# Performance work log

Hardware: AMD Instinct MI355X
Metric: run time of the kernel (lower is better)

## Reference

```python
import jax, jax.numpy as jnp
import numpy as np

B, T, V, D, F, L, H = 2, 1024, 50257, 768, 3072, 6, 12
HD = D // H
EPS = 1e-5


def setup_inputs() -> dict:
    key = jax.random.key(0)
    ks = jax.random.split(key, 8)
    s = 0.02
    return {
        "idx": jax.random.randint(ks[0], (B, T), 0, V),
        "tok_emb": jax.random.normal(ks[1], (V, D), jnp.float32) * s,
        "pos_emb": jax.random.normal(ks[2], (T, D), jnp.float32) * s,
        "ln1_w": jnp.ones((L, D), jnp.float32),
        "ln1_b": jnp.zeros((L, D), jnp.float32),
        "qkv_w": jax.random.normal(ks[3], (L, 3 * D, D), jnp.float32) * s,
        "qkv_b": jnp.zeros((L, 3 * D), jnp.float32),
        "out_w": jax.random.normal(ks[4], (L, D, D), jnp.float32) * s,
        "out_b": jnp.zeros((L, D), jnp.float32),
        "ln2_w": jnp.ones((L, D), jnp.float32),
        "ln2_b": jnp.zeros((L, D), jnp.float32),
        "fc1_w": jax.random.normal(ks[5], (L, F, D), jnp.float32) * s,
        "fc1_b": jnp.zeros((L, F), jnp.float32),
        "fc2_w": jax.random.normal(ks[6], (L, D, F), jnp.float32) * s,
        "fc2_b": jnp.zeros((L, D), jnp.float32),
        "lnf_w": jnp.ones((D,), jnp.float32),
        "lnf_b": jnp.zeros((D,), jnp.float32),
    }


def _ln(x, w, b):
    m = x.mean(-1, keepdims=True)
    v = ((x - m) ** 2).mean(-1, keepdims=True)
    return (x - m) * jax.lax.rsqrt(v + EPS) * w + b


def reference(idx, tok_emb, pos_emb, ln1_w, ln1_b, qkv_w, qkv_b, out_w, out_b,
              ln2_w, ln2_b, fc1_w, fc1_b, fc2_w, fc2_b, lnf_w, lnf_b):
    b, t = idx.shape
    x = tok_emb[idx] + pos_emb[:t]  # (B,T,D)
    mask = jnp.tril(jnp.ones((t, t), bool))
    scale = HD ** -0.5

    def block(x, p):
        l1w, l1b, qw, qb, ow, ob, l2w, l2b, f1w, f1b, f2w, f2b = p
        h = _ln(x, l1w, l1b)
        qkv = h @ qw.T + qb                     # (B,T,3D)
        q, k, v = jnp.split(qkv, 3, axis=-1)
        q = q.reshape(b, t, H, HD).transpose(0, 2, 1, 3)  # (B,H,T,HD)
        k = k.reshape(b, t, H, HD).transpose(0, 2, 1, 3)
        v = v.reshape(b, t, H, HD).transpose(0, 2, 1, 3)
        attn = jnp.einsum('bhqd,bhkd->bhqk', q, k) * scale
        attn = jnp.where(mask, attn, -jnp.inf)
        attn = jax.nn.softmax(attn, axis=-1)
        o = jnp.einsum('bhqk,bhkd->bhqd', attn, v)
        o = o.transpose(0, 2, 1, 3).reshape(b, t, D)
        x = x + o @ ow.T + ob
        h = _ln(x, l2w, l2b)
        x = x + jax.nn.gelu(h @ f1w.T + f1b, approximate=False) @ f2w.T + f2b
        return x, None

    x, _ = jax.lax.scan(block, x, (ln1_w, ln1_b, qkv_w, qkv_b, out_w, out_b,
                                   ln2_w, ln2_b, fc1_w, fc1_b, fc2_w, fc2_b))
    x = _ln(x, lnf_w, lnf_b)
    logits = x @ tok_emb.T  # weight-tied head, (B,T,V)
    return logits
```

## Files before the change

kernel.cpp:

```cpp
#include <hip/hip_runtime.h>
#include <hip/hip_bf16.h>

typedef __attribute__((ext_vector_type(8))) short short8;
typedef __attribute__((ext_vector_type(4))) float f32x4;
typedef __attribute__((ext_vector_type(4))) unsigned short u16x4;

#define DEVI static __device__ __forceinline__

constexpr int TT  = 1024;
constexpr int DD  = 768;
constexpr int FF  = 3072;
constexpr int VV  = 50257;
constexpr int VP  = 50304;
constexpr int HH  = 12;
constexpr int BTOT = 2048;

DEVI unsigned short f2bf(float f) {
    unsigned int u = __builtin_bit_cast(unsigned int, f);
    u += 0x7fffu + ((u >> 16) & 1u);
    return (unsigned short)(u >> 16);
}
DEVI float bf2f(unsigned short h) {
    unsigned int u = ((unsigned int)h) << 16;
    return __builtin_bit_cast(float, u);
}
DEVI f32x4 mfma16(short8 a, short8 b, f32x4 c) {
    return __builtin_amdgcn_mfma_f32_16x16x32_bf16(a, b, c, 0, 0, 0);
}

__global__ __launch_bounds__(256) void cvt4_k(const float* __restrict__ s,
                                              unsigned short* __restrict__ d, long n4) {
    long i = (long)blockIdx.x * 256 + threadIdx.x;
    if (i >= n4) return;
    float4 v = ((const float4*)s)[i];
    u16x4 o;
    o[0] = f2bf(v.x); o[1] = f2bf(v.y); o[2] = f2bf(v.z); o[3] = f2bf(v.w);
    ((u16x4*)d)[i] = o;
}

__global__ __launch_bounds__(192) void pad_tok_k(const float* __restrict__ s,
                                                 unsigned short* __restrict__ d) {
    int r = blockIdx.x;
    int c = threadIdx.x * 4;
    u16x4 o = {0, 0, 0, 0};
    if (r < VV) {
        float4 v = *(const float4*)(s + (size_t)r * DD + c);
        o[0] = f2bf(v.x); o[1] = f2bf(v.y); o[2] = f2bf(v.z); o[3] = f2bf(v.w);
    }
    *(u16x4*)(d + (size_t)r * DD + c) = o;
}

__global__ __launch_bounds__(256) void embed_k(const int* __restrict__ idx,
                                               const float* __restrict__ tok,
                                               const float* __restrict__ pos,
                                               float* __restrict__ x) {
    int row = blockIdx.x;
    int t = row & (TT - 1);
    int id = idx[row];
    for (int c = threadIdx.x; c < DD; c += 256)
        x[(size_t)row * DD + c] = tok[(size_t)id * DD + c] + pos[(size_t)t * DD + c];
}

__global__ __launch_bounds__(256) void ln_k(const float* __restrict__ x,
                                            const float* __restrict__ w,
                                            const float* __restrict__ b,
                                            unsigned short* __restrict__ out) {
    int row = blockIdx.x;
    const float* xr = x + (size_t)row * DD;
    int tid = threadIdx.x;
    float v0 = xr[tid], v1 = xr[tid + 256], v2 = xr[tid + 512];
    float s = v0 + v1 + v2;
    #pragma unroll
    for (int m = 1; m < 64; m <<= 1) s += __shfl_xor(s, m);
    __shared__ float red[8];
    int wv = tid >> 6, ln = tid & 63;
    if (ln == 0) red[wv] = s;
    __syncthreads();
    float mean = (red[0] + red[1] + red[2] + red[3]) * (1.f / 768.f);
    float d0 = v0 - mean, d1 = v1 - mean, d2 = v2 - mean;
    float sq = d0 * d0 + d1 * d1 + d2 * d2;
    #pragma unroll
    for (int m = 1; m < 64; m <<= 1) sq += __shfl_xor(sq, m);
    if (ln == 0) red[4 + wv] = sq;
    __syncthreads();
    float var = (red[4] + red[5] + red[6] + red[7]) * (1.f / 768.f);
    float rstd = rsqrtf(var + 1e-5f);
    out[(size_t)row * DD + tid]       = f2bf(d0 * rstd * w[tid]       + b[tid]);
    out[(size_t)row * DD + tid + 256] = f2bf(d1 * rstd * w[tid + 256] + b[tid + 256]);
    out[(size_t)row * DD + tid + 512] = f2bf(d2 * rstd * w[tid + 512] + b[tid + 512]);
}

template<int EPI>
__global__ __launch_bounds__(256) void gemm_bt(const unsigned short* __restrict__ A,
                                               const unsigned short* __restrict__ B,
                                               const float* __restrict__ bias,
                                               float* __restrict__ Cf,
                                               unsigned short* __restrict__ Cb,
                                               int M, int N, int K, int ldc, int Nreal) {
    __shared__ __align__(16) unsigned short As[128 * 32];
    __shared__ __align__(16) unsigned short Bs[128 * 32];
    const int tid = threadIdx.x;
    const int wave = tid >> 6, lane = tid & 63;
    const int m0 = blockIdx.y * 128, n0 = blockIdx.x * 128;
    const int wm = wave >> 1, wn = wave & 1;
    const int g = lane >> 4, r16 = lane & 15;

    f32x4 acc[4][4] = {};

    const int srow = wave * 32 + (lane >> 2);
    const int scol = (lane & 3) * 8;
    const unsigned short* Aptr = A + (size_t)(m0 + srow) * K + scol;
    const unsigned short* Bptr = B + (size_t)(n0 + srow) * K + scol;

    const int nsteps = K >> 5;
    for (int kt = 0; kt < nsteps; ++kt) {
        const int k0 = kt << 5;
        #pragma unroll
        for (int i = 0; i < 2; i++) {
            __builtin_amdgcn_global_load_lds(
                (const __attribute__((address_space(1))) void*)(Aptr + (size_t)i * 16 * K + k0),
                (__attribute__((address_space(3))) void*)(As + (wave * 2 + i) * 512),
                16, 0, 0);
        }
        #pragma unroll
        for (int i = 0; i < 2; i++) {
            __builtin_amdgcn_global_load_lds(
                (const __attribute__((address_space(1))) void*)(Bptr + (size_t)i * 16 * K + k0),
                (__attribute__((address_space(3))) void*)(Bs + (wave * 2 + i) * 512),
                16, 0, 0);
        }
        asm volatile("s_waitcnt vmcnt(0)" ::: "memory");
        __syncthreads();
        short8 af[4], bfr[4];
        #pragma unroll
        for (int m = 0; m < 4; m++)
            af[m] = *(const short8*)&As[(wm * 64 + m * 16 + r16) * 32 + g * 8];
        #pragma unroll
        for (int n = 0; n < 4; n++)
            bfr[n] = *(const short8*)&Bs[(wn * 64 + n * 16 + r16) * 32 + g * 8];
        #pragma unroll
        for (int m = 0; m < 4; m++)
            #pragma unroll
            for (int n = 0; n < 4; n++)
                acc[m][n] = mfma16(af[m], bfr[n], acc[m][n]);
        __syncthreads();
    }

    #pragma unroll
    for (int n = 0; n < 4; n++) {
        int gcol = n0 + wn * 64 + n * 16 + r16;
        float bv = (EPI == 3) ? 0.f : bias[gcol];
        #pragma unroll
        for (int m = 0; m < 4; m++) {
            int grow0 = m0 + wm * 64 + m * 16 + g * 4;
            #pragma unroll
            for (int r = 0; r < 4; r++) {
                float v = acc[m][n][r] + bv;
                size_t off = (size_t)(grow0 + r) * ldc + gcol;
                if (EPI == 0) {
                    Cb[off] = f2bf(v);
                } else if (EPI == 1) {
                    float ge = 0.5f * v * (1.f + erff(v * 0.70710678118654752f));
                    Cb[off] = f2bf(ge);
                } else if (EPI == 2) {
                    Cf[off] = Cf[off] + v;
                } else {
                    if (gcol < Nreal) Cf[off] = v;
                }
            }
        }
    }
}

__global__ __launch_bounds__(256) void vtrans_k(const unsigned short* __restrict__ qkv,
                                                unsigned short* __restrict__ vT) {
    int bh = blockIdx.y;
    int b = bh / HH, h = bh - b * HH;
    int t0 = blockIdx.x * 64;
    __shared__ unsigned short tile[64][65];
    int tid = threadIdx.x;
    int dl = tid & 63, tq = tid >> 6;
    #pragma unroll
    for (int i = 0; i < 16; i++) {
        int tl = i * 4 + tq;
        tile[tl][dl] = qkv[(size_t)(b * TT + t0 + tl) * (3 * DD) + 2 * DD + h * 64 + dl];
    }
    __syncthreads();
    #pragma unroll
    for (int i = 0; i < 16; i++) {
        int d2 = i * 4 + tq;
        vT[((size_t)bh * 64 + d2) * TT + t0 + dl] = tile[dl][d2];
    }
}

__global__ __launch_bounds__(256) void attn_k(const unsigned short* __restrict__ qkv,
                                              const unsigned short* __restrict__ vT,
                                              unsigned short* __restrict__ out) {
    const int w = threadIdx.x >> 6, lane = threadIdx.x & 63;
    const int g = lane >> 4, r16 = lane & 15;
    const int qt = blockIdx.x, bh = blockIdx.y;
    const int b = bh / HH, h = bh - b * HH;
    __shared__ __align__(16) unsigned short Plds[4 * 1280];
    const int qbase = qt * 64 + w * 16;

    short8 aq[2];
    #pragma unroll
    for (int kk = 0; kk < 2; kk++)
        aq[kk] = *(const short8*)(qkv + (size_t)(b * TT + qbase + r16) * (3 * DD)
                                  + h * 64 + kk * 32 + g * 8);

    f32x4 oacc[4] = {};
    float mrow[4], lrow[4];
    #pragma unroll
    for (int r = 0; r < 4; r++) { mrow[r] = -1e30f; lrow[r] = 0.f; }

    for (int kt = 0; kt <= qt; ++kt) {
        f32x4 sacc[4] = {};
        #pragma unroll
        for (int j = 0; j < 4; j++) {
            #pragma unroll
            for (int kk = 0; kk < 2; kk++) {
                short8 bk = *(const short8*)(qkv + (size_t)(b * TT + kt * 64 + j * 16 + r16) * (3 * DD)
                                             + DD + h * 64 + kk * 32 + g * 8);
                sacc[j] = mfma16(aq[kk], bk, sacc[j]);
            }
        }
        const bool diag = (kt == qt);
        float s[4][4], pm[4];
        #pragma unroll
        for (int r = 0; r < 4; r++) pm[r] = -1e30f;
        #pragma unroll
        for (int j = 0; j < 4; j++) {
            int kcol = kt * 64 + j * 16 + r16;
            #pragma unroll
            for (int r = 0; r < 4; r++) {
                float v = sacc[j][r] * 0.125f;
                if (diag && kcol > qbase + g * 4 + r) v = -1e30f;
                s[j][r] = v;
                pm[r] = fmaxf(pm[r], v);
            }
        }
        #pragma unroll
        for (int r = 0; r < 4; r++) {
            #pragma unroll
            for (int msk = 1; msk < 16; msk <<= 1)
                pm[r] = fmaxf(pm[r], __shfl_xor(pm[r], msk));
        }
        float cf[4], rs[4];
        #pragma unroll
        for (int r = 0; r < 4; r++) {
            float mn = fmaxf(mrow[r], pm[r]);
            cf[r] = __expf(mrow[r] - mn);
            mrow[r] = mn;
            rs[r] = 0.f;
        }
        #pragma unroll
        for (int j = 0; j < 4; j++)
            #pragma unroll
            for (int r = 0; r < 4; r++) {
                float p = __expf(s[j][r] - mrow[r]);
                s[j][r] = p;
                rs[r] += p;
            }
        #pragma unroll
        for (int r = 0; r < 4; r++) {
            #pragma unroll
            for (int msk = 1; msk < 16; msk <<= 1) rs[r] += __shfl_xor(rs[r], msk);
            lrow[r] = lrow[r] * cf[r] + rs[r];
        }
        #pragma unroll
        for (int jd = 0; jd < 4; jd++)
            #pragma unroll
            for (int r = 0; r < 4; r++) oacc[jd][r] *= cf[r];

        asm volatile("s_waitcnt lgkmcnt(0)" ::: "memory");
        #pragma unroll
        for (int j = 0; j < 4; j++)
            #pragma unroll
            for (int r = 0; r < 4; r++)
                Plds[w * 1280 + (g * 4 + r) * 80 + j * 16 + r16] = f2bf(s[j][r]);
        asm volatile("s_waitcnt lgkmcnt(0)" ::: "memory");
        short8 ap[2];
        #pragma unroll
        for (int kk = 0; kk < 2; kk++)
            ap[kk] = *(const short8*)&Plds[w * 1280 + r16 * 80 + kk * 32 + g * 8];
        #pragma unroll
        for (int jd = 0; jd < 4; jd++) {
            #pragma unroll
            for (int kk = 0; kk < 2; kk++) {
                short8 bv = *(const short8*)(vT + ((size_t)bh * 64 + jd * 16 + r16) * TT
                                             + kt * 64 + kk * 32 + g * 8);
                oacc[jd] = mfma16(ap[kk], bv, oacc[jd]);
            }
        }
    }
    #pragma unroll
    for (int jd = 0; jd < 4; jd++) {
        int d = h * 64 + jd * 16 + r16;
        #pragma unroll
        for (int r = 0; r < 4; r++) {
            int t = qbase + g * 4 + r;
            out[(size_t)(b * TT + t) * DD + d] = f2bf(oacc[jd][r] / lrow[r]);
        }
    }
}

#define OFF_X    0u
#define OFF_H    (6291456u)
#define OFF_QKV  (OFF_H   + 3145728u)
#define OFF_VT   (OFF_QKV + 9437184u)
#define OFF_ATT  (OFF_VT  + 3145728u)
#define OFF_GEL  (OFF_ATT + 3145728u)
#define OFF_WQ   (OFF_GEL + 12582912u)
#define OFF_WO   (OFF_WQ  + 21233664u)
#define OFF_WF1  (OFF_WO  + 7077888u)
#define OFF_WF2  (OFF_WF1 + 28311552u)
#define OFF_TOK  (OFF_WF2 + 28311552u)

extern "C" void kernel_launch(void* const* d_in, const int* in_sizes, int n_in,
                              void* d_out, int out_size, void* d_ws, size_t ws_size,
                              hipStream_t stream) {
    const int*   idx  = (const int*)  d_in[0];
    const float* tok  = (const float*)d_in[1];
    const float* pos  = (const float*)d_in[2];
    const float* ln1w = (const float*)d_in[3];
    const float* ln1b = (const float*)d_in[4];
    const float* qkvw = (const float*)d_in[5];
    const float* qkvb = (const float*)d_in[6];
    const float* outw = (const float*)d_in[7];
    const float* outb = (const float*)d_in[8];
    const float* ln2w = (const float*)d_in[9];
    const float* ln2b = (const float*)d_in[10];
    const float* fc1w = (const float*)d_in[11];
    const float* fc1b = (const float*)d_in[12];
    const float* fc2w = (const float*)d_in[13];
    const float* fc2b = (const float*)d_in[14];
    const float* lnfw = (const float*)d_in[15];
    const float* lnfb = (const float*)d_in[16];

    char* ws = (char*)d_ws;
    float*          x    = (float*)         (ws + OFF_X);
    unsigned short* hbuf = (unsigned short*)(ws + OFF_H);
    unsigned short* qkvB = (unsigned short*)(ws + OFF_QKV);
    unsigned short* vT   = (unsigned short*)(ws + OFF_VT);
    unsigned short* attB = (unsigned short*)(ws + OFF_ATT);
    unsigned short* gelB = (unsigned short*)(ws + OFF_GEL);
    unsigned short* wq   = (unsigned short*)(ws + OFF_WQ);
    unsigned short* wo   = (unsigned short*)(ws + OFF_WO);
    unsigned short* wf1  = (unsigned short*)(ws + OFF_WF1);
    unsigned short* wf2  = (unsigned short*)(ws + OFF_WF2);
    unsigned short* tokp = (unsigned short*)(ws + OFF_TOK);

    cvt4_k<<<10368, 256, 0, stream>>>(qkvw, wq,  (long)6 * 2304 * 768 / 4);
    cvt4_k<<<3456,  256, 0, stream>>>(outw, wo,  (long)6 * 768  * 768 / 4);
    cvt4_k<<<13824, 256, 0, stream>>>(fc1w, wf1, (long)6 * 3072 * 768 / 4);
    cvt4_k<<<13824, 256, 0, stream>>>(fc2w, wf2, (long)6 * 768  * 3072 / 4);
    pad_tok_k<<<VP, 192, 0, stream>>>(tok, tokp);

    embed_k<<<BTOT, 256, 0, stream>>>(idx, tok, pos, x);

    for (int l = 0; l < 6; l++) {
        ln_k<<<BTOT, 256, 0, stream>>>(x, ln1w + l * DD, ln1b + l * DD, hbuf);
        gemm_bt<0><<<dim3(18, 16), 256, 0, stream>>>(hbuf, wq + (size_t)l * 2304 * 768,
                                                     qkvb + l * 2304, nullptr, qkvB,
                                                     BTOT, 2304, 768, 2304, 2304);
        vtrans_k<<<dim3(16, 24), 256, 0, stream>>>(qkvB, vT);
        attn_k<<<dim3(16, 24), 256, 0, stream>>>(qkvB, vT, attB);
        gemm_bt<2><<<dim3(6, 16), 256, 0, stream>>>(attB, wo + (size_t)l * 768 * 768,
                                                    outb + l * DD, x, nullptr,
                                                    BTOT, 768, 768, 768, 768);
        ln_k<<<BTOT, 256, 0, stream>>>(x, ln2w + l * DD, ln2b + l * DD, hbuf);
        gemm_bt<1><<<dim3(24, 16), 256, 0, stream>>>(hbuf, wf1 + (size_t)l * 3072 * 768,
                                                     fc1b + l * FF, nullptr, gelB,
                                                     BTOT, 3072, 768, 3072, 3072);
        gemm_bt<2><<<dim3(6, 16), 256, 0, stream>>>(gelB, wf2 + (size_t)l * 768 * 3072,
                                                    fc2b + l * DD, x, nullptr,
                                                    BTOT, 768, 3072, 768, 768);
    }
    ln_k<<<BTOT, 256, 0, stream>>>(x, lnfw, lnfb, hbuf);
    gemm_bt<3><<<dim3(VP / 128, 16), 256, 0, stream>>>(hbuf, tokp, nullptr,
                                                       (float*)d_out, nullptr,
                                                       BTOT, VP, 768, VV, VV);
}
```

Before: 2.466 ms.

## Use 64x64 tiles for narrow GEMMs and XCD-swizzle the LM head grid

The out-projection and fc2 GEMMs (N=768) now use a new 64x64-tile kernel launched on a 12x32 grid instead of 6x16 blocks of 128x128. This gives more blocks to fill the CUs. The LM head GEMM uses a 1-D grid remapped so each XCD processes a contiguous range of vocab column blocks across all row blocks, aiming for better L2 reuse of the token-embedding weights. The vocab padding grows to 51200 to make that mapping divide evenly, which adds some wasted compute and requires a larger padded buffer. The smaller tiles also lower per-block data reuse.

```diff
diff --git a/kernel.cpp b/kernel.cpp
--- a/kernel.cpp
+++ b/kernel.cpp
@@ -11,7 +11,7 @@
 constexpr int DD  = 768;
 constexpr int FF  = 3072;
 constexpr int VV  = 50257;
-constexpr int VP  = 50304;
+constexpr int VP2 = 51200;
 constexpr int HH  = 12;
 constexpr int BTOT = 2048;
 
@@ -90,7 +90,7 @@
     out[(size_t)row * DD + tid + 512] = f2bf(d2 * rstd * w[tid + 512] + b[tid + 512]);
 }
 
-template<int EPI>
+template<int EPI, bool XSW>
 __global__ __launch_bounds__(256) void gemm_bt(const unsigned short* __restrict__ A,
                                                const unsigned short* __restrict__ B,
                                                const float* __restrict__ bias,
@@ -101,7 +101,18 @@
     __shared__ __align__(16) unsigned short Bs[128 * 32];
     const int tid = threadIdx.x;
     const int wave = tid >> 6, lane = tid & 63;
-    const int m0 = blockIdx.y * 128, n0 = blockIdx.x * 128;
+    int m0, n0;
+    if (XSW) {
+        int lid = blockIdx.x;
+        int xcd = lid & 7;
+        int per = lid >> 3;
+        int mb  = per & 15;
+        int nper = N >> 10;
+        int nb  = xcd * nper + (per >> 4);
+        m0 = mb << 7; n0 = nb << 7;
+    } else {
+        m0 = blockIdx.y * 128; n0 = blockIdx.x * 128;
+    }
     const int wm = wave >> 1, wn = wave & 1;
     const int g = lane >> 4, r16 = lane & 15;
 
@@ -167,6 +178,70 @@
                 } else {
                     if (gcol < Nreal) Cf[off] = v;
                 }
+            }
+        }
+    }
+}
+
+__global__ __launch_bounds__(256) void gemm64_bt(const unsigned short* __restrict__ A,
+                                                 const unsigned short* __restrict__ B,
+                                                 const float* __restrict__ bias,
+                                                 float* __restrict__ Cf,
+                                                 int M, int N, int K, int ldc) {
+    __shared__ __align__(16) unsigned short As[64 * 32];
+    __shared__ __align__(16) unsigned short Bs[64 * 32];
+    const int tid = threadIdx.x;
+    const int wave = tid >> 6, lane = tid & 63;
+    const int m0 = blockIdx.y * 64, n0 = blockIdx.x * 64;
+    const int wm = wave >> 1, wn = wave & 1;
+    const int g = lane >> 4, r16 = lane & 15;
+
+    f32x4 acc[2][2] = {};
+
+    const int srow = wave * 16 + (lane >> 2);
+    const int scol = (lane & 3) * 8;
+    const unsigned short* Aptr = A + (size_t)(m0 + srow) * K + scol;
+    const unsigned short* Bptr = B + (size_t)(n0 + srow) * K + scol;
+
+    const int nsteps = K >> 5;
+    for (int kt = 0; kt < nsteps; ++kt) {
+        const int k0 = kt << 5;
+        __builtin_amdgcn_global_load_lds(
+            (const __attribute__((address_space(1))) void*)(Aptr + k0),
+            (__attribute__((address_space(3))) void*)(As + wave * 512),
+            16, 0, 0);
+        __builtin_amdgcn_global_load_lds(
+            (const __attribute__((address_space(1))) void*)(Bptr + k0),
+            (__attribute__((address_space(3))) void*)(Bs + wave * 512),
+            16, 0, 0);
+        asm volatile("s_waitcnt vmcnt(0)" ::: "memory");
+        __syncthreads();
+        short8 af[2], bfr[2];
+        #pragma unroll
+        for (int m = 0; m < 2; m++)
+            af[m] = *(const short8*)&As[(wm * 32 + m * 16 + r16) * 32 + g * 8];
+        #pragma unroll
+        for (int n = 0; n < 2; n++)
+            bfr[n] = *(const short8*)&Bs[(wn * 32 + n * 16 + r16) * 32 + g * 8];
+        #pragma unroll
+        for (int m = 0; m < 2; m++)
+            #pragma unroll
+            for (int n = 0; n < 2; n++)
+                acc[m][n] = mfma16(af[m], bfr[n], acc[m][n]);
+        __syncthreads();
+    }
+
+    #pragma unroll
+    for (int n = 0; n < 2; n++) {
+        int gcol = n0 + wn * 32 + n * 16 + r16;
+        float bv = bias[gcol];
+        #pragma unroll
+        for (int m = 0; m < 2; m++) {
+            int grow0 = m0 + wm * 32 + m * 16 + g * 4;
+            #pragma unroll
+            for (int r = 0; r < 4; r++) {
+                size_t off = (size_t)(grow0 + r) * ldc + gcol;
+                Cf[off] = Cf[off] + acc[m][n][r] + bv;
             }
         }
     }
@@ -355,30 +430,30 @@
     cvt4_k<<<3456,  256, 0, stream>>>(outw, wo,  (long)6 * 768  * 768 / 4);
     cvt4_k<<<13824, 256, 0, stream>>>(fc1w, wf1, (long)6 * 3072 * 768 / 4);
     cvt4_k<<<13824, 256, 0, stream>>>(fc2w, wf2, (long)6 * 768  * 3072 / 4);
-    pad_tok_k<<<VP, 192, 0, stream>>>(tok, tokp);
+    pad_tok_k<<<VP2, 192, 0, stream>>>(tok, tokp);
 
     embed_k<<<BTOT, 256, 0, stream>>>(idx, tok, pos, x);
 
     for (int l = 0; l < 6; l++) {
         ln_k<<<BTOT, 256, 0, stream>>>(x, ln1w + l * DD, ln1b + l * DD, hbuf);
-        gemm_bt<0><<<dim3(18, 16), 256, 0, stream>>>(hbuf, wq + (size_t)l * 2304 * 768,
+        gemm_bt<0, false><<<dim3(18, 16), 256, 0, stream>>>(hbuf, wq + (size_t)l * 2304 * 768,
                                                      qkvb + l * 2304, nullptr, qkvB,
                                                      BTOT, 2304, 768, 2304, 2304);
         vtrans_k<<<dim3(16, 24), 256, 0, stream>>>(qkvB, vT);
         attn_k<<<dim3(16, 24), 256, 0, stream>>>(qkvB, vT, attB);
-        gemm_bt<2><<<dim3(6, 16), 256, 0, stream>>>(attB, wo + (size_t)l * 768 * 768,
-                                                    outb + l * DD, x, nullptr,
-                                                    BTOT, 768, 768, 768, 768);
+        gemm64_bt<<<dim3(12, 32), 256, 0, stream>>>(attB, wo + (size_t)l * 768 * 768,
+                                                    outb + l * DD, x,
+                                                    BTOT, 768, 768, 768);
         ln_k<<<BTOT, 256, 0, stream>>>(x, ln2w + l * DD, ln2b + l * DD, hbuf);
-        gemm_bt<1><<<dim3(24, 16), 256, 0, stream>>>(hbuf, wf1 + (size_t)l * 3072 * 768,
+        gemm_bt<1, false><<<dim3(24, 16), 256, 0, stream>>>(hbuf, wf1 + (size_t)l * 3072 * 768,
                                                      fc1b + l * FF, nullptr, gelB,
                                                      BTOT, 3072, 768, 3072, 3072);
-        gemm_bt<2><<<dim3(6, 16), 256, 0, stream>>>(gelB, wf2 + (size_t)l * 768 * 3072,
-                                                    fc2b + l * DD, x, nullptr,
-                                                    BTOT, 768, 3072, 768, 768);
+        gemm64_bt<<<dim3(12, 32), 256, 0, stream>>>(gelB, wf2 + (size_t)l * 768 * 3072,
+                                                    fc2b + l * DD, x,
+                                                    BTOT, 768, 3072, 768);
     }
     ln_k<<<BTOT, 256, 0, stream>>>(x, lnfw, lnfb, hbuf);
-    gemm_bt<3><<<dim3(VP / 128, 16), 256, 0, stream>>>(hbuf, tokp, nullptr,
+    gemm_bt<3, true><<<dim3(16 * (VP2 / 128), 1), 256, 0, stream>>>(hbuf, tokp, nullptr,
                                                        (float*)d_out, nullptr,
-                                                       BTOT, VP, 768, VV, VV);
-}
+                                                       BTOT, VP2, 768, VV, VV);
+}
```

Result: faster. 2.170 ms (-12.0%).
